# Performance work log

Measured on AMD Instinct MI355X. Metric: run time of the kernel, lower is better.

## Reference

```python
import jax, jax.numpy as jnp
import numpy as np

N = 50000        # nodes
E = 1_600_000    # edges (avg degree 32)
F_IN = 128       # num_features
H = 128          # hidden_size
C = 10           # num_classes
EPS = 1e-12      # F.normalize eps


def _glorot(key, fan_in, fan_out):
    lim = np.sqrt(6.0 / (fan_in + fan_out)).astype(np.float32)
    return jax.random.uniform(key, (fan_in, fan_out), jnp.float32, -lim, lim)


def setup_inputs() -> dict:
    key = jax.random.key(0)
    ks = jax.random.split(key, 12)
    x = jax.random.normal(ks[0], (N, F_IN), jnp.float32)
    edge_index = jax.random.randint(ks[1], (2, E), 0, N, dtype=jnp.int64)
    edge_weights = jax.random.uniform(ks[2], (E,), jnp.float32)
    W1 = _glorot(ks[3], F_IN, H); b1 = jnp.zeros((H,), jnp.float32)
    W2 = _glorot(ks[4], H, H);    b2 = jnp.zeros((H,), jnp.float32)
    W3 = _glorot(ks[5], H, H);    b3 = jnp.zeros((H,), jnp.float32)
    Wlin = _glorot(ks[6], 3 * H, C)
    blin = jnp.zeros((C,), jnp.float32)
    return {"x": x, "edge_index": edge_index, "edge_weights": edge_weights,
            "W1": W1, "b1": b1, "W2": W2, "b2": b2, "W3": W3, "b3": b3,
            "Wlin": Wlin, "blin": blin}


def _gcn_conv(x, W, b, src, dst, w, dinv):
    # h = X W ; out[dst] += (dinv[src]*w*dinv[dst]) * h[src] ; + bias
    h = x @ W                                     # [N, H]
    coef = dinv[src] * w * dinv[dst]              # [E+N]
    agg = jax.ops.segment_sum(h[src] * coef[:, None], dst, num_segments=N)
    return agg + b


def _l2_relu(x):
    n = jnp.sqrt(jnp.sum(x * x, axis=1, keepdims=True))
    return jax.nn.relu(x / jnp.maximum(n, EPS))


def reference(x, edge_index, edge_weights, W1, b1, W2, b2, W3, b3, Wlin, blin):
    # add self-loops with weight 1 (PyG GCNConv default)
    loop = jnp.arange(N, dtype=edge_index.dtype)
    src = jnp.concatenate([edge_index[0], loop])
    dst = jnp.concatenate([edge_index[1], loop])
    w = jnp.concatenate([edge_weights, jnp.ones((N,), edge_weights.dtype)])
    # symmetric normalization from destination-side degree
    deg = jax.ops.segment_sum(w, dst, num_segments=N)
    dinv = jnp.where(deg > 0, jax.lax.rsqrt(deg), 0.0)

    out1 = _l2_relu(_gcn_conv(x, W1, b1, src, dst, w, dinv))
    out2 = _l2_relu(_gcn_conv(out1, W2, b2, src, dst, w, dinv))
    out3 = _l2_relu(_gcn_conv(out2, W3, b3, src, dst, w, dinv))
    rep = jnp.concatenate([out1, out2, out3], axis=1)   # [N, 3H]
    return rep @ Wlin + blin                             # [N, C]
```

## Files before the change

kernel.cpp:

```cpp
#include <hip/hip_runtime.h>
#include <hip/hip_fp16.h>

#define N_NODES 50000
#define N_EDGES 1600000
#define FDIM    128
#define C_OUT   10
#define NBLK    ((N_NODES + 255) / 256)

typedef unsigned long long u64;
typedef unsigned int u32;
typedef unsigned short u16;
#define FX_BITS 44
#define FX_MASK ((1ull << FX_BITS) - 1)
#define FX_SCALE 4294967296.0

__device__ __forceinline__ u32 pack_h2(float a, float b) {
    __half2 h = __floats2half2_rn(a, b);
    return *(u32*)&h;
}
__device__ __forceinline__ float2 unpack_h2(u32 u) {
    __half2 h = *(__half2*)&u;
    return __half22float2(h);
}
__device__ __forceinline__ u32 pack_edge(int s, float c) {
    __half h = __float2half_rn(c);
    u16 hb = *(u16*)&h;
    return ((u32)s << 15) | (u32)hb;
}
__device__ __forceinline__ int edge_src(u32 u) { return (int)(u >> 15); }
__device__ __forceinline__ float edge_coef(u32 u) {
    u16 hb = (u16)(u & 0x7FFFu);
    __half h = *(__half*)&hb;
    return __half2float(h);
}

__global__ void k_init(u64* __restrict__ hist) {
    int i = blockIdx.x * 256 + threadIdx.x;
    if (i < N_NODES) hist[i] = 0ull;
}

__global__ void k_hist(const int* __restrict__ dst, const float* __restrict__ w,
                       u64* __restrict__ hist) {
    int e = blockIdx.x * 256 + threadIdx.x;
    if (e < N_EDGES) {
        u64 fx = (u64)((double)w[e] * FX_SCALE + 0.5);
        u64 packed = (1ull << FX_BITS) | fx;
        atomicAdd(&hist[dst[e]], packed);
    }
}

__global__ __launch_bounds__(256)
void k_scan1(const u64* __restrict__ hist, int* __restrict__ blocksum) {
    int i = blockIdx.x * 256 + threadIdx.x;
    int v = (i < N_NODES) ? (int)(hist[i] >> FX_BITS) : 0;
#pragma unroll
    for (int off = 32; off >= 1; off >>= 1) v += __shfl_xor(v, off, 64);
    __shared__ int ws[4];
    if ((threadIdx.x & 63) == 0) ws[threadIdx.x >> 6] = v;
    __syncthreads();
    if (threadIdx.x == 0) blocksum[blockIdx.x] = ws[0] + ws[1] + ws[2] + ws[3];
}

__global__ __launch_bounds__(256)
void k_scan2(int* __restrict__ blocksum) {
    int t = threadIdx.x, lane = t & 63, w = t >> 6;
    int v = (t < NBLK) ? blocksum[t] : 0;
    int x = v;
#pragma unroll
    for (int off = 1; off < 64; off <<= 1) {
        int y = __shfl_up(x, off, 64);
        if (lane >= off) x += y;
    }
    __shared__ int ws[4];
    if (lane == 63) ws[w] = x;
    __syncthreads();
    int add = 0;
    for (int j = 0; j < w; ++j) add += ws[j];
    if (t < NBLK) blocksum[t] = add + x - v;
}

__global__ __launch_bounds__(256)
void k_scan3(const u64* __restrict__ hist, const int* __restrict__ blocksum,
             float* __restrict__ dinv, int* __restrict__ cursor,
             int* __restrict__ rowptr) {
    int i = blockIdx.x * 256 + threadIdx.x;
    int t = threadIdx.x, lane = t & 63, w = t >> 6;
    u64 hv = (i < N_NODES) ? hist[i] : 0ull;
    int v = (int)(hv >> FX_BITS);
    int x = v;
#pragma unroll
    for (int off = 1; off < 64; off <<= 1) {
        int y = __shfl_up(x, off, 64);
        if (lane >= off) x += y;
    }
    __shared__ int ws[4];
    if (lane == 63) ws[w] = x;
    __syncthreads();
    int add = blocksum[blockIdx.x];
    for (int j = 0; j < w; ++j) add += ws[j];
    int excl = add + x - v;
    if (i < N_NODES) {
        rowptr[i] = excl;
        cursor[i] = excl;
        float dg = 1.0f + (float)((double)(hv & FX_MASK) * (1.0 / FX_SCALE));
        dinv[i] = rsqrtf(dg);
        if (i == N_NODES - 1) rowptr[N_NODES] = N_EDGES;
    }
}

__global__ void k_scatter(const int* __restrict__ src, const int* __restrict__ dst,
                          const float* __restrict__ w, const float* __restrict__ dinv,
                          int* __restrict__ cursor, u32* __restrict__ edat) {
    int e = blockIdx.x * 256 + threadIdx.x;
    if (e < N_EDGES) {
        int s = src[e], d = dst[e];
        int pos = atomicAdd(&cursor[d], 1);
        float c = dinv[s] * w[e] * dinv[d];
        __builtin_nontemporal_store(pack_edge(s, c), &edat[pos]);
    }
}

template<typename TIN>
__global__ __launch_bounds__(256)
void k_gemm(const TIN* __restrict__ X, const float* __restrict__ W,
            u16* __restrict__ H) {
    __shared__ float Wl[64][128];
    __shared__ float Xl[64][68];
    int t = threadIdx.x;
    int rb = blockIdx.x * 64;
    int colb = (t & 31) * 4;
    int rg = t >> 5;

    float acc[8][4] = {};

    for (int k0 = 0; k0 < 128; k0 += 64) {
        {
            const float4* Wg = (const float4*)(W + k0 * 128);
            float4* Ws = (float4*)&Wl[0][0];
#pragma unroll
            for (int j = 0; j < 8; ++j) Ws[t + 256 * j] = Wg[t + 256 * j];
        }
        {
#pragma unroll
            for (int j = 0; j < 4; ++j) {
                int idx = t + 256 * j;
                int r = idx >> 4;
                int c4 = (idx & 15) * 4;
                int row = rb + r;
                float4 v = make_float4(0.f, 0.f, 0.f, 0.f);
                if (row < N_NODES) {
                    if constexpr (sizeof(TIN) == 4) {
                        v = *(const float4*)(X + (size_t)row * FDIM + k0 + c4);
                    } else {
                        uint2 pv = *(const uint2*)(X + (size_t)row * FDIM + k0 + c4);
                        float2 lo = unpack_h2(pv.x), hi = unpack_h2(pv.y);
                        v = make_float4(lo.x, lo.y, hi.x, hi.y);
                    }
                }
                *(float4*)&Xl[r][c4] = v;
            }
        }
        __syncthreads();
#pragma unroll
        for (int k = 0; k < 64; k += 4) {
            float4 wv0 = *(const float4*)&Wl[k + 0][colb];
            float4 wv1 = *(const float4*)&Wl[k + 1][colb];
            float4 wv2 = *(const float4*)&Wl[k + 2][colb];
            float4 wv3 = *(const float4*)&Wl[k + 3][colb];
#pragma unroll
            for (int r = 0; r < 8; ++r) {
                float4 xv = *(const float4*)&Xl[rg * 8 + r][k];
                acc[r][0] += xv.x * wv0.x; acc[r][1] += xv.x * wv0.y;
                acc[r][2] += xv.x * wv0.z; acc[r][3] += xv.x * wv0.w;
                acc[r][0] += xv.y * wv1.x; acc[r][1] += xv.y * wv1.y;
                acc[r][2] += xv.y * wv1.z; acc[r][3] += xv.y * wv1.w;
                acc[r][0] += xv.z * wv2.x; acc[r][1] += xv.z * wv2.y;
                acc[r][2] += xv.z * wv2.z; acc[r][3] += xv.z * wv2.w;
                acc[r][0] += xv.w * wv3.x; acc[r][1] += xv.w * wv3.y;
                acc[r][2] += xv.w * wv3.z; acc[r][3] += xv.w * wv3.w;
            }
        }
        __syncthreads();
    }
#pragma unroll
    for (int r = 0; r < 8; ++r) {
        int row = rb + rg * 8 + r;
        if (row < N_NODES) {
            uint2 pv;
            pv.x = pack_h2(acc[r][0], acc[r][1]);
            pv.y = pack_h2(acc[r][2], acc[r][3]);
            *(uint2*)(H + (size_t)row * FDIM + colb) = pv;
        }
    }
}

__global__ __launch_bounds__(256)
void k_agg(const u16* __restrict__ H, const int* __restrict__ rowptr,
           const u32* __restrict__ edat, const float* __restrict__ dinv,
           const float* __restrict__ bias, u32* __restrict__ out) {
    int wid  = threadIdx.x >> 6;
    int lane = threadIdx.x & 63;
    int node = blockIdx.x * 4 + wid;
    if (node >= N_NODES) return;

    const u32* H2 = (const u32*)H;
    float di = dinv[node];
    float2 acc;
    {
        float2 hv = unpack_h2(H2[(size_t)node * 64 + lane]);
        float cs = di * di;
        acc.x = cs * hv.x; acc.y = cs * hv.y;
    }
    int e = rowptr[node], eend = rowptr[node + 1];
    for (; e + 4 <= eend; e += 4) {
        u32 e0 = edat[e], e1 = edat[e + 1], e2 = edat[e + 2], e3 = edat[e + 3];
        u32 r0 = H2[(size_t)edge_src(e0) * 64 + lane];
        u32 r1 = H2[(size_t)edge_src(e1) * 64 + lane];
        u32 r2 = H2[(size_t)edge_src(e2) * 64 + lane];
        u32 r3 = H2[(size_t)edge_src(e3) * 64 + lane];
        float2 v0 = unpack_h2(r0), v1 = unpack_h2(r1);
        float2 v2 = unpack_h2(r2), v3 = unpack_h2(r3);
        float c0 = edge_coef(e0), c1 = edge_coef(e1);
        float c2 = edge_coef(e2), c3 = edge_coef(e3);
        acc.x += c0 * v0.x; acc.y += c0 * v0.y;
        acc.x += c1 * v1.x; acc.y += c1 * v1.y;
        acc.x += c2 * v2.x; acc.y += c2 * v2.y;
        acc.x += c3 * v3.x; acc.y += c3 * v3.y;
    }
    for (; e < eend; ++e) {
        u32 ed = edat[e];
        float c = edge_coef(ed);
        float2 v = unpack_h2(H2[(size_t)edge_src(ed) * 64 + lane]);
        acc.x += c * v.x; acc.y += c * v.y;
    }
    acc.x += bias[lane * 2];
    acc.y += bias[lane * 2 + 1];

    float ss = acc.x * acc.x + acc.y * acc.y;
#pragma unroll
    for (int off = 32; off >= 1; off >>= 1) ss += __shfl_xor(ss, off, 64);
    float n = sqrtf(ss);
    float inv = 1.0f / fmaxf(n, 1e-12f);
    float ox = fmaxf(acc.x * inv, 0.0f);
    float oy = fmaxf(acc.y * inv, 0.0f);
    out[(size_t)node * 64 + lane] = pack_h2(ox, oy);
}

__global__ __launch_bounds__(256)
void k_final(const u32* __restrict__ o1, const u32* __restrict__ o2,
             const u32* __restrict__ o3, const float* __restrict__ Wlin,
             const float* __restrict__ blin, float* __restrict__ out) {
    __shared__ float Wt[C_OUT][384];
    __shared__ float part[4][8][C_OUT];
    __shared__ float bl[C_OUT];
    int t = threadIdx.x;
    for (int i = t; i < 384 * C_OUT; i += 256) {
        int f = i / C_OUT, c = i % C_OUT;
        Wt[c][f] = Wlin[i];
    }
    if (t < C_OUT) bl[t] = blin[t];
    __syncthreads();

    int wid = t >> 6, lane = t & 63;
    int node = blockIdx.x * 4 + wid;

    float2 va = unpack_h2(o1[(size_t)node * 64 + lane]);
    float2 vb = unpack_h2(o2[(size_t)node * 64 + lane]);
    float2 vc = unpack_h2(o3[(size_t)node * 64 + lane]);
    int f0 = lane * 2;

    float acc[C_OUT];
#pragma unroll
    for (int c = 0; c < C_OUT; ++c) {
        acc[c] = va.x * Wt[c][f0]       + va.y * Wt[c][f0 + 1]
               + vb.x * Wt[c][128 + f0] + vb.y * Wt[c][129 + f0]
               + vc.x * Wt[c][256 + f0] + vc.y * Wt[c][257 + f0];
    }
#pragma unroll
    for (int off = 32; off >= 8; off >>= 1)
#pragma unroll
        for (int c = 0; c < C_OUT; ++c) acc[c] += __shfl_xor(acc[c], off, 64);

    if (lane < 8) {
#pragma unroll
        for (int c = 0; c < C_OUT; ++c) part[wid][lane][c] = acc[c];
    }
    __syncthreads();
    if (t < 4 * C_OUT) {
        int n = t / C_OUT, cc = t % C_OUT;
        float s = 0.f;
#pragma unroll
        for (int l = 0; l < 8; ++l) s += part[n][l][cc];
        out[(size_t)(blockIdx.x * 4 + n) * C_OUT + cc] = s + bl[cc];
    }
}

extern "C" void kernel_launch(void* const* d_in, const int* in_sizes, int n_in,
                              void* d_out, int out_size, void* d_ws, size_t ws_size,
                              hipStream_t stream) {
    const float* x  = (const float*)d_in[0];
    const int*   ei = (const int*)d_in[1];
    const float* ew = (const float*)d_in[2];
    const float* W1 = (const float*)d_in[3];
    const float* b1 = (const float*)d_in[4];
    const float* W2 = (const float*)d_in[5];
    const float* b2 = (const float*)d_in[6];
    const float* W3 = (const float*)d_in[7];
    const float* b3 = (const float*)d_in[8];
    const float* Wl = (const float*)d_in[9];
    const float* bl = (const float*)d_in[10];
    float* out = (float*)d_out;

    const int* srcI = ei;
    const int* dstI = ei + N_EDGES;

    char* p = (char*)d_ws;
    auto alloc = [&](size_t bytes) {
        char* r = p;
        p += (bytes + 255) & ~(size_t)255;
        return r;
    };
    u64*   hist   = (u64*)  alloc((size_t)N_NODES * 8);
    float* dinv   = (float*)alloc((size_t)N_NODES * 4);
    int*   cursor = (int*)  alloc((size_t)N_NODES * 4);
    int*   rowptr = (int*)  alloc((size_t)(N_NODES + 1) * 4);
    int*   bsum   = (int*)  alloc((size_t)NBLK * 4);
    u32*   edat   = (u32*)  alloc((size_t)N_EDGES * 4);
    u16*   h      = (u16*)  alloc((size_t)N_NODES * FDIM * 2);
    u32*   o1     = (u32*)  alloc((size_t)N_NODES * 64 * 4);
    u32*   o2     = (u32*)  alloc((size_t)N_NODES * 64 * 4);
    u32*   o3     = (u32*)  alloc((size_t)N_NODES * 64 * 4);

    k_init   <<<NBLK, 256, 0, stream>>>(hist);
    k_hist   <<<(N_EDGES + 255) / 256, 256, 0, stream>>>(dstI, ew, hist);
    k_scan1  <<<NBLK, 256, 0, stream>>>(hist, bsum);
    k_scan2  <<<1, 256, 0, stream>>>(bsum);
    k_scan3  <<<NBLK, 256, 0, stream>>>(hist, bsum, dinv, cursor, rowptr);
    k_scatter<<<(N_EDGES + 255) / 256, 256, 0, stream>>>(srcI, dstI, ew, dinv, cursor, edat);

    u32* outs[3] = {o1, o2, o3};
    const float* bvecs[3] = {b1, b2, b3};

    k_gemm<float><<<(N_NODES + 63) / 64, 256, 0, stream>>>(x, W1, h);
    k_agg<<<N_NODES / 4, 256, 0, stream>>>(h, rowptr, edat, dinv, bvecs[0], outs[0]);
    k_gemm<u16><<<(N_NODES + 63) / 64, 256, 0, stream>>>((const u16*)outs[0], W2, h);
    k_agg<<<N_NODES / 4, 256, 0, stream>>>(h, rowptr, edat, dinv, bvecs[1], outs[1]);
    k_gemm<u16><<<(N_NODES + 63) / 64, 256, 0, stream>>>((const u16*)outs[1], W3, h);
    k_agg<<<N_NODES / 4, 256, 0, stream>>>(h, rowptr, edat, dinv, bvecs[2], outs[2]);

    k_final<<<N_NODES / 4, 256, 0, stream>>>(o1, o2, o3, Wl, bl, out);
}
```

Baseline: 592.5 us.

## Build CSR via two-level bucket partition and fold dinv into GEMM epilogue

Graph preprocessing now builds the CSR in two passes. Edges are first partitioned into 128-node buckets with shared-memory histograms and a single bucket scan. Each bucket is then sorted locally in shared memory, which also computes degree and dinv. This replaces per-node global atomics on a 64-bit histogram and a random scatter with a per-edge global atomic cursor. The symmetric normalization is factored: the GEMM output is pre-scaled by dinv[src], the edge stores the raw weight, and the aggregation multiplies by dinv[dst] at the end. The cost is an extra 8-byte staging buffer and a fixed-point degree sum with lower precision (2^20 scale).

```diff
diff --git a/kernel.cpp b/kernel.cpp
--- a/kernel.cpp
+++ b/kernel.cpp
@@ -5,14 +5,16 @@
 #define N_EDGES 1600000
 #define FDIM    128
 #define C_OUT   10
-#define NBLK    ((N_NODES + 255) / 256)
+
+#define EBLK   8192
+#define PBLK   ((N_EDGES + EBLK - 1) / EBLK)
+#define BSHIFT 7
+#define BNODES 128
+#define NB     ((N_NODES + BNODES - 1) / BNODES)
 
 typedef unsigned long long u64;
 typedef unsigned int u32;
 typedef unsigned short u16;
-#define FX_BITS 44
-#define FX_MASK ((1ull << FX_BITS) - 1)
-#define FX_SCALE 4294967296.0
 
 __device__ __forceinline__ u32 pack_h2(float a, float b) {
     __half2 h = __floats2half2_rn(a, b);
@@ -22,108 +24,163 @@
     __half2 h = *(__half2*)&u;
     return __half22float2(h);
 }
-__device__ __forceinline__ u32 pack_edge(int s, float c) {
-    __half h = __float2half_rn(c);
+__device__ __forceinline__ u32 pack_edge(int s, float w) {
+    __half h = __float2half_rn(w);
     u16 hb = *(u16*)&h;
     return ((u32)s << 15) | (u32)hb;
 }
 __device__ __forceinline__ int edge_src(u32 u) { return (int)(u >> 15); }
-__device__ __forceinline__ float edge_coef(u32 u) {
+__device__ __forceinline__ float edge_w(u32 u) {
     u16 hb = (u16)(u & 0x7FFFu);
     __half h = *(__half*)&hb;
     return __half2float(h);
 }
-
-__global__ void k_init(u64* __restrict__ hist) {
-    int i = blockIdx.x * 256 + threadIdx.x;
-    if (i < N_NODES) hist[i] = 0ull;
-}
-
-__global__ void k_hist(const int* __restrict__ dst, const float* __restrict__ w,
-                       u64* __restrict__ hist) {
-    int e = blockIdx.x * 256 + threadIdx.x;
-    if (e < N_EDGES) {
-        u64 fx = (u64)((double)w[e] * FX_SCALE + 0.5);
-        u64 packed = (1ull << FX_BITS) | fx;
-        atomicAdd(&hist[dst[e]], packed);
-    }
-}
-
-__global__ __launch_bounds__(256)
-void k_scan1(const u64* __restrict__ hist, int* __restrict__ blocksum) {
-    int i = blockIdx.x * 256 + threadIdx.x;
-    int v = (i < N_NODES) ? (int)(hist[i] >> FX_BITS) : 0;
-#pragma unroll
-    for (int off = 32; off >= 1; off >>= 1) v += __shfl_xor(v, off, 64);
-    __shared__ int ws[4];
-    if ((threadIdx.x & 63) == 0) ws[threadIdx.x >> 6] = v;
-    __syncthreads();
-    if (threadIdx.x == 0) blocksum[blockIdx.x] = ws[0] + ws[1] + ws[2] + ws[3];
-}
-
-__global__ __launch_bounds__(256)
-void k_scan2(int* __restrict__ blocksum) {
-    int t = threadIdx.x, lane = t & 63, w = t >> 6;
-    int v = (t < NBLK) ? blocksum[t] : 0;
+__device__ __forceinline__ u64 pack_stage(int dl, int s, float w) {
+    return ((u64)(u32)dl << 56) | ((u64)(u32)s << 32) | (u64)__float_as_uint(w);
+}
+
+__global__ void k_zero(u32* __restrict__ bucketCnt) {
+    int t = threadIdx.x;
+    if (t < NB) bucketCnt[t] = 0;
+}
+
+__global__ __launch_bounds__(256)
+void k_bhist(const int* __restrict__ dst, u32* __restrict__ bucketCnt) {
+    __shared__ u32 cnt[NB];
+    int t = threadIdx.x;
+    for (int i = t; i < NB; i += 256) cnt[i] = 0;
+    __syncthreads();
+    int e0 = blockIdx.x * EBLK;
+    for (int i = t; i < EBLK; i += 256) {
+        int e = e0 + i;
+        if (e < N_EDGES) atomicAdd(&cnt[dst[e] >> BSHIFT], 1u);
+    }
+    __syncthreads();
+    for (int i = t; i < NB; i += 256)
+        if (cnt[i]) atomicAdd(&bucketCnt[i], cnt[i]);
+}
+
+__global__ __launch_bounds__(512)
+void k_bscan(const u32* __restrict__ bucketCnt, int* __restrict__ bucketBase,
+             int* __restrict__ bucketCursor, int* __restrict__ rowptr) {
+    int t = threadIdx.x, lane = t & 63, wv = t >> 6;
+    int v = (t < NB) ? (int)bucketCnt[t] : 0;
     int x = v;
 #pragma unroll
     for (int off = 1; off < 64; off <<= 1) {
         int y = __shfl_up(x, off, 64);
         if (lane >= off) x += y;
     }
-    __shared__ int ws[4];
-    if (lane == 63) ws[w] = x;
+    __shared__ int wt[8];
+    if (lane == 63) wt[wv] = x;
     __syncthreads();
     int add = 0;
-    for (int j = 0; j < w; ++j) add += ws[j];
-    if (t < NBLK) blocksum[t] = add + x - v;
-}
-
-__global__ __launch_bounds__(256)
-void k_scan3(const u64* __restrict__ hist, const int* __restrict__ blocksum,
-             float* __restrict__ dinv, int* __restrict__ cursor,
-             int* __restrict__ rowptr) {
-    int i = blockIdx.x * 256 + threadIdx.x;
-    int t = threadIdx.x, lane = t & 63, w = t >> 6;
-    u64 hv = (i < N_NODES) ? hist[i] : 0ull;
-    int v = (int)(hv >> FX_BITS);
-    int x = v;
-#pragma unroll
-    for (int off = 1; off < 64; off <<= 1) {
-        int y = __shfl_up(x, off, 64);
-        if (lane >= off) x += y;
-    }
-    __shared__ int ws[4];
-    if (lane == 63) ws[w] = x;
-    __syncthreads();
-    int add = blocksum[blockIdx.x];
-    for (int j = 0; j < w; ++j) add += ws[j];
-    int excl = add + x - v;
-    if (i < N_NODES) {
-        rowptr[i] = excl;
-        cursor[i] = excl;
-        float dg = 1.0f + (float)((double)(hv & FX_MASK) * (1.0 / FX_SCALE));
-        dinv[i] = rsqrtf(dg);
-        if (i == N_NODES - 1) rowptr[N_NODES] = N_EDGES;
-    }
-}
-
-__global__ void k_scatter(const int* __restrict__ src, const int* __restrict__ dst,
-                          const float* __restrict__ w, const float* __restrict__ dinv,
-                          int* __restrict__ cursor, u32* __restrict__ edat) {
-    int e = blockIdx.x * 256 + threadIdx.x;
-    if (e < N_EDGES) {
-        int s = src[e], d = dst[e];
-        int pos = atomicAdd(&cursor[d], 1);
-        float c = dinv[s] * w[e] * dinv[d];
-        __builtin_nontemporal_store(pack_edge(s, c), &edat[pos]);
+    for (int j = 0; j < wv; ++j) add += wt[j];
+    if (t < NB) {
+        int excl = add + x - v;
+        bucketBase[t]   = excl;
+        bucketCursor[t] = excl;
+    }
+    if (t == 0) {
+        bucketBase[NB]     = N_EDGES;
+        rowptr[N_NODES]    = N_EDGES;
+    }
+}
+
+__global__ __launch_bounds__(256)
+void k_part(const int* __restrict__ src, const int* __restrict__ dst,
+            const float* __restrict__ w, int* __restrict__ bucketCursor,
+            u64* __restrict__ staging) {
+    __shared__ u32 cnt[NB];
+    __shared__ u32 base[NB];
+    __shared__ u32 lcur[NB];
+    int t = threadIdx.x;
+    for (int i = t; i < NB; i += 256) cnt[i] = 0;
+    __syncthreads();
+    int e0 = blockIdx.x * EBLK;
+    for (int i = t; i < EBLK; i += 256) {
+        int e = e0 + i;
+        if (e < N_EDGES) atomicAdd(&cnt[dst[e] >> BSHIFT], 1u);
+    }
+    __syncthreads();
+    for (int i = t; i < NB; i += 256) {
+        u32 c = cnt[i];
+        lcur[i] = 0;
+        if (c) base[i] = (u32)atomicAdd(&bucketCursor[i], (int)c);
+    }
+    __syncthreads();
+    for (int i = t; i < EBLK; i += 256) {
+        int e = e0 + i;
+        if (e >= N_EDGES) continue;
+        int d = dst[e];
+        int b = d >> BSHIFT;
+        u32 pos = base[b] + atomicAdd(&lcur[b], 1u);
+        staging[pos] = pack_stage(d & (BNODES - 1), src[e], w[e]);
+    }
+}
+
+__global__ __launch_bounds__(256)
+void k_build(const u64* __restrict__ staging, const int* __restrict__ bucketBase,
+             int* __restrict__ rowptr, float* __restrict__ dinv,
+             u32* __restrict__ edat) {
+    __shared__ u32 cnt[BNODES];
+    __shared__ u32 wfx[BNODES];
+    __shared__ int rowl[BNODES];
+    __shared__ u32 cur[BNODES];
+    __shared__ int wt[2];
+    int t = threadIdx.x;
+    int b = blockIdx.x;
+    int lo = b * BNODES;
+    int nn = min(BNODES, N_NODES - lo);
+    int segBase = bucketBase[b], segEnd = bucketBase[b + 1];
+
+    if (t < BNODES) { cnt[t] = 0; wfx[t] = 0; }
+    __syncthreads();
+    for (int i = segBase + t; i < segEnd; i += 256) {
+        u64 r = staging[i];
+        int d = (int)(r >> 56);
+        float wv = __uint_as_float((u32)r);
+        atomicAdd(&cnt[d], 1u);
+        atomicAdd(&wfx[d], (u32)(wv * 1048576.0f + 0.5f));
+    }
+    __syncthreads();
+    int v = 0, x = 0, lane = t & 63, wv2 = t >> 6;
+    if (t < BNODES) {
+        v = (int)cnt[t]; x = v;
+#pragma unroll
+        for (int off = 1; off < 64; off <<= 1) {
+            int y = __shfl_up(x, off, 64);
+            if (lane >= off) x += y;
+        }
+        if (lane == 63) wt[wv2] = x;
+    }
+    __syncthreads();
+    if (t < BNODES) {
+        int add = (wv2 == 1) ? wt[0] : 0;
+        int ro = add + x - v;
+        rowl[t] = ro;
+        cur[t]  = 0;
+        if (t < nn) {
+            rowptr[lo + t] = segBase + ro;
+            float deg = 1.0f + (float)wfx[t] * (1.0f / 1048576.0f);
+            dinv[lo + t] = rsqrtf(deg);
+        }
+    }
+    __syncthreads();
+    for (int i = segBase + t; i < segEnd; i += 256) {
+        u64 r = staging[i];
+        int d = (int)(r >> 56);
+        int s = (int)((r >> 32) & 0x1FFFF);
+        float wf = __uint_as_float((u32)r);
+        u32 slot = (u32)rowl[d] + atomicAdd(&cur[d], 1u);
+        edat[segBase + slot] = pack_edge(s, wf);
     }
 }
 
 template<typename TIN>
 __global__ __launch_bounds__(256)
 void k_gemm(const TIN* __restrict__ X, const float* __restrict__ W,
-            u16* __restrict__ H) {
+            const float* __restrict__ dinv, u16* __restrict__ H) {
     __shared__ float Wl[64][128];
     __shared__ float Xl[64][68];
     int t = threadIdx.x;
@@ -147,17 +204,17 @@
                 int r = idx >> 4;
                 int c4 = (idx & 15) * 4;
                 int row = rb + r;
-                float4 v = make_float4(0.f, 0.f, 0.f, 0.f);
+                float4 vv = make_float4(0.f, 0.f, 0.f, 0.f);
                 if (row < N_NODES) {
                     if constexpr (sizeof(TIN) == 4) {
-                        v = *(const float4*)(X + (size_t)row * FDIM + k0 + c4);
+                        vv = *(const float4*)(X + (size_t)row * FDIM + k0 + c4);
                     } else {
                         uint2 pv = *(const uint2*)(X + (size_t)row * FDIM + k0 + c4);
-                        float2 lo = unpack_h2(pv.x), hi = unpack_h2(pv.y);
-                        v = make_float4(lo.x, lo.y, hi.x, hi.y);
+                        float2 lov = unpack_h2(pv.x), hiv = unpack_h2(pv.y);
+                        vv = make_float4(lov.x, lov.y, hiv.x, hiv.y);
                     }
                 }
-                *(float4*)&Xl[r][c4] = v;
+                *(float4*)&Xl[r][c4] = vv;
             }
         }
         __syncthreads();
@@ -186,9 +243,10 @@
     for (int r = 0; r < 8; ++r) {
         int row = rb + rg * 8 + r;
         if (row < N_NODES) {
+            float di = dinv[row];
             uint2 pv;
-            pv.x = pack_h2(acc[r][0], acc[r][1]);
-            pv.y = pack_h2(acc[r][2], acc[r][3]);
+            pv.x = pack_h2(acc[r][0] * di, acc[r][1] * di);
+            pv.y = pack_h2(acc[r][2] * di, acc[r][3] * di);
             *(uint2*)(H + (size_t)row * FDIM + colb) = pv;
         }
     }
@@ -205,12 +263,8 @@
 
     const u32* H2 = (const u32*)H;
     float di = dinv[node];
-    float2 acc;
-    {
-        float2 hv = unpack_h2(H2[(size_t)node * 64 + lane]);
-        float cs = di * di;
-        acc.x = cs * hv.x; acc.y = cs * hv.y;
-    }
+    float2 acc = unpack_h2(H2[(size_t)node * 64 + lane]);
+
     int e = rowptr[node], eend = rowptr[node + 1];
     for (; e + 4 <= eend; e += 4) {
         u32 e0 = edat[e], e1 = edat[e + 1], e2 = edat[e + 2], e3 = edat[e + 3];
@@ -220,8 +274,8 @@
         u32 r3 = H2[(size_t)edge_src(e3) * 64 + lane];
         float2 v0 = unpack_h2(r0), v1 = unpack_h2(r1);
         float2 v2 = unpack_h2(r2), v3 = unpack_h2(r3);
-        float c0 = edge_coef(e0), c1 = edge_coef(e1);
-        float c2 = edge_coef(e2), c3 = edge_coef(e3);
+        float c0 = edge_w(e0), c1 = edge_w(e1);
+        float c2 = edge_w(e2), c3 = edge_w(e3);
         acc.x += c0 * v0.x; acc.y += c0 * v0.y;
         acc.x += c1 * v1.x; acc.y += c1 * v1.y;
         acc.x += c2 * v2.x; acc.y += c2 * v2.y;
@@ -229,12 +283,12 @@
     }
     for (; e < eend; ++e) {
         u32 ed = edat[e];
-        float c = edge_coef(ed);
-        float2 v = unpack_h2(H2[(size_t)edge_src(ed) * 64 + lane]);
-        acc.x += c * v.x; acc.y += c * v.y;
-    }
-    acc.x += bias[lane * 2];
-    acc.y += bias[lane * 2 + 1];
+        float c = edge_w(ed);
+        float2 vv = unpack_h2(H2[(size_t)edge_src(ed) * 64 + lane]);
+        acc.x += c * vv.x; acc.y += c * vv.y;
+    }
+    acc.x = acc.x * di + bias[lane * 2];
+    acc.y = acc.y * di + bias[lane * 2 + 1];
 
     float ss = acc.x * acc.x + acc.y * acc.y;
 #pragma unroll
@@ -320,33 +374,30 @@
         p += (bytes + 255) & ~(size_t)255;
         return r;
     };
-    u64*   hist   = (u64*)  alloc((size_t)N_NODES * 8);
-    float* dinv   = (float*)alloc((size_t)N_NODES * 4);
-    int*   cursor = (int*)  alloc((size_t)N_NODES * 4);
-    int*   rowptr = (int*)  alloc((size_t)(N_NODES + 1) * 4);
-    int*   bsum   = (int*)  alloc((size_t)NBLK * 4);
-    u32*   edat   = (u32*)  alloc((size_t)N_EDGES * 4);
-    u16*   h      = (u16*)  alloc((size_t)N_NODES * FDIM * 2);
-    u32*   o1     = (u32*)  alloc((size_t)N_NODES * 64 * 4);
-    u32*   o2     = (u32*)  alloc((size_t)N_NODES * 64 * 4);
-    u32*   o3     = (u32*)  alloc((size_t)N_NODES * 64 * 4);
-
-    k_init   <<<NBLK, 256, 0, stream>>>(hist);
-    k_hist   <<<(N_EDGES + 255) / 256, 256, 0, stream>>>(dstI, ew, hist);
-    k_scan1  <<<NBLK, 256, 0, stream>>>(hist, bsum);
-    k_scan2  <<<1, 256, 0, stream>>>(bsum);
-    k_scan3  <<<NBLK, 256, 0, stream>>>(hist, bsum, dinv, cursor, rowptr);
-    k_scatter<<<(N_EDGES + 255) / 256, 256, 0, stream>>>(srcI, dstI, ew, dinv, cursor, edat);
-
-    u32* outs[3] = {o1, o2, o3};
-    const float* bvecs[3] = {b1, b2, b3};
-
-    k_gemm<float><<<(N_NODES + 63) / 64, 256, 0, stream>>>(x, W1, h);
-    k_agg<<<N_NODES / 4, 256, 0, stream>>>(h, rowptr, edat, dinv, bvecs[0], outs[0]);
-    k_gemm<u16><<<(N_NODES + 63) / 64, 256, 0, stream>>>((const u16*)outs[0], W2, h);
-    k_agg<<<N_NODES / 4, 256, 0, stream>>>(h, rowptr, edat, dinv, bvecs[1], outs[1]);
-    k_gemm<u16><<<(N_NODES + 63) / 64, 256, 0, stream>>>((const u16*)outs[1], W3, h);
-    k_agg<<<N_NODES / 4, 256, 0, stream>>>(h, rowptr, edat, dinv, bvecs[2], outs[2]);
+    u32*   bucketCnt  = (u32*)alloc((size_t)NB * 4);
+    int*   bucketBase = (int*)alloc((size_t)(NB + 1) * 4);
+    int*   bucketCur  = (int*)alloc((size_t)NB * 4);
+    int*   rowptr     = (int*)alloc((size_t)(N_NODES + 1) * 4);
+    float* dinv       = (float*)alloc((size_t)N_NODES * 4);
+    u64*   staging    = (u64*)alloc((size_t)N_EDGES * 8);
+    u32*   edat       = (u32*)alloc((size_t)N_EDGES * 4);
+    u16*   h          = (u16*)alloc((size_t)N_NODES * FDIM * 2);
+    u32*   o1         = (u32*)alloc((size_t)N_NODES * 64 * 4);
+    u32*   o2         = (u32*)alloc((size_t)N_NODES * 64 * 4);
+    u32*   o3         = (u32*)alloc((size_t)N_NODES * 64 * 4);
+
+    k_zero <<<1, 512, 0, stream>>>(bucketCnt);
+    k_bhist<<<PBLK, 256, 0, stream>>>(dstI, bucketCnt);
+    k_bscan<<<1, 512, 0, stream>>>(bucketCnt, bucketBase, bucketCur, rowptr);
+    k_part <<<PBLK, 256, 0, stream>>>(srcI, dstI, ew, bucketCur, staging);
+    k_build<<<NB, 256, 0, stream>>>(staging, bucketBase, rowptr, dinv, edat);
+
+    k_gemm<float><<<(N_NODES + 63) / 64, 256, 0, stream>>>(x, W1, dinv, h);
+    k_agg<<<N_NODES / 4, 256, 0, stream>>>(h, rowptr, edat, dinv, b1, o1);
+    k_gemm<u16><<<(N_NODES + 63) / 64, 256, 0, stream>>>((const u16*)o1, W2, dinv, h);
+    k_agg<<<N_NODES / 4, 256, 0, stream>>>(h, rowptr, edat, dinv, b2, o2);
+    k_gemm<u16><<<(N_NODES + 63) / 64, 256, 0, stream>>>((const u16*)o2, W3, dinv, h);
+    k_agg<<<N_NODES / 4, 256, 0, stream>>>(h, rowptr, edat, dinv, b3, o3);
 
     k_final<<<N_NODES / 4, 256, 0, stream>>>(o1, o2, o3, Wl, bl, out);
 }
```

After: 494.3 us. 1.2x faster.
